# Kernel optimization log

Measured on AMD Instinct MI355X. Metric: run time of the kernel, lower is better.

The kernel has to match this reference:

```python
import jax, jax.numpy as jnp
import numpy as np

_CODESZ = 8   # E8 codeword dimension
_OFFSET = 0.25  # half-integer shift applied to D8 points


def _build_grid():
    # Faithful replication of get_grid(): cartesian product of arange(-4,4)
    # over 8 dims (torch.cartesian_prod order == 'ij' meshgrid, last dim fastest),
    # keep points with even coordinate sum and squared norm <= 10 (D8 subset),
    # then concat [d8 - 1/4, d8 + 1/4]. Yields 55650 codewords of dim 8.
    rng = np.arange(-4, 4, dtype=np.int8)
    pts = np.stack(np.meshgrid(*([rng] * _CODESZ), indexing='ij'), axis=-1).reshape(-1, _CODESZ)
    s = pts.sum(axis=-1, dtype=np.int16)
    n2 = (pts.astype(np.int16) * pts).sum(axis=-1)  # max 8*16 fits int16
    d8 = pts[(s % 2 == 0) & (n2 <= 10)].astype(np.float32)  # [27825, 8]
    grid = np.concatenate([d8 - _OFFSET, d8 + _OFFSET], axis=0)  # [55650, 8]
    grid_norm = (grid * grid).sum(axis=-1)  # diag(grid @ grid.T), [55650]
    return jnp.asarray(grid), jnp.asarray(grid_norm)


def setup_inputs() -> dict:
    key = jax.random.key(0)
    X = jax.random.normal(key, (8192, _CODESZ), dtype=jnp.float32)
    grid, grid_norm = _build_grid()
    return {"X": X, "grid": grid, "grid_norm": grid_norm}


def reference(X, grid, grid_norm):
    # quantize(X, return_idx=True):
    # nearest codeword under L2 <=> argmax of 2*X@g - ||g||^2
    scores = 2.0 * (X @ grid.T) - grid_norm          # [N, 55650]
    idx = jnp.argmax(scores, axis=-1)                # [N]
    vals = jnp.take(grid, idx, axis=0)               # [N, 8]
    idx_i16 = (idx + (-2 ** 15)).astype(jnp.int16)   # idx_offset + int16 cast
    return vals, idx_i16
```

## Files before the change

### kernel.cpp

```cpp
#include <hip/hip_runtime.h>
#include <math.h>


typedef short short8 __attribute__((ext_vector_type(8)));
typedef float f32x16 __attribute__((ext_vector_type(16)));

constexpr int NROWS  = 8192;
constexpr int NCW    = 55650;
constexpr int NT     = 1740;
constexpr int NCWP   = NT * 32;
constexpr int NCHUNK = 32;
constexpr int RBLK   = 32;

constexpr size_t OFF_GB = 0;
constexpr size_t OFF_XS = OFF_GB + (size_t)NCWP * 32;
constexpr size_t OFF_BK = OFF_XS + (size_t)NROWS * 64;

__device__ inline unsigned short bf16_rne(float f) {
  unsigned int u = __float_as_uint(f);
  unsigned int r = u + 0x7FFFu + ((u >> 16) & 1u);
  return (unsigned short)(r >> 16);
}
__device__ inline float bf16_f(unsigned short h) {
  return __uint_as_float(((unsigned int)h) << 16);
}
__device__ inline unsigned int enc_ord(float f) {
  unsigned int u = __float_as_uint(f);
  return (u & 0x80000000u) ? ~u : (u | 0x80000000u);
}
__device__ inline float dec_ord(unsigned int e) {
  unsigned int u = (e & 0x80000000u) ? (e & 0x7FFFFFFFu) : ~e;
  return __uint_as_float(u);
}
__device__ inline float max16(const f32x16& d) {
  float t1 = fmaxf(fmaxf(d[0], d[1]), d[2]);
  float t2 = fmaxf(fmaxf(d[3], d[4]), d[5]);
  float t3 = fmaxf(fmaxf(d[6], d[7]), d[8]);
  float t4 = fmaxf(fmaxf(d[9], d[10]), d[11]);
  float t5 = fmaxf(fmaxf(d[12], d[13]), d[14]);
  float u1 = fmaxf(fmaxf(t1, t2), t3);
  float u2 = fmaxf(fmaxf(t4, t5), d[15]);
  return fmaxf(u1, u2);
}

__global__ __launch_bounds__(256) void e8_prep(
    const float* __restrict__ X, const float* __restrict__ G,
    const float* __restrict__ GN, unsigned short* __restrict__ Gb,
    unsigned short* __restrict__ Xs, unsigned long long* __restrict__ best) {
  int i = blockIdx.x * 256 + threadIdx.x;
  if (i < NCWP) {
    unsigned short g16[16];
    if (i < NCW) {
      for (int j = 0; j < 8; ++j) g16[j] = bf16_rne(G[(size_t)i*8+j]);
      g16[8] = bf16_rne(GN[i]);
      for (int j = 9; j < 16; ++j) g16[j] = 0;
    } else {
      for (int j = 0; j < 8; ++j) g16[j] = 0;
      g16[8] = 0x7F7F;
      for (int j = 9; j < 16; ++j) g16[j] = 0;
    }
    uint4* dst = reinterpret_cast<uint4*>(Gb + (size_t)i * 16);
    dst[0] = *reinterpret_cast<uint4*>(&g16[0]);
    dst[1] = *reinterpret_cast<uint4*>(&g16[8]);
  } else if (i < NCWP + NROWS) {
    int r = i - NCWP;
    unsigned short hh[8], mm[8], ll[8], qq[8];
    for (int j = 0; j < 8; ++j) {
      float s = 2.0f * X[(size_t)r*8+j];
      unsigned short h = bf16_rne(s);  float r1 = s  - bf16_f(h);
      unsigned short m = bf16_rne(r1); float r2 = r1 - bf16_f(m);
      unsigned short l = bf16_rne(r2);
      hh[j] = h; mm[j] = m; ll[j] = l;
      qq[j] = (j == 0) ? (unsigned short)0xBF80 : 0;
    }
    uint4* dst = reinterpret_cast<uint4*>(Xs + (size_t)r * 32);
    dst[0] = *reinterpret_cast<uint4*>(hh);
    dst[1] = *reinterpret_cast<uint4*>(mm);
    dst[2] = *reinterpret_cast<uint4*>(ll);
    dst[3] = *reinterpret_cast<uint4*>(qq);
    best[r] = 0ull;
  }
}

__global__ __launch_bounds__(256, 4) void e8_main(
    const unsigned short* __restrict__ Gb,
    const unsigned short* __restrict__ Xs,
    unsigned long long* __restrict__ best) {
  const int lane = threadIdx.x & 63;
  const int wave = threadIdx.x >> 6;
  const int kg = lane >> 5, l31 = lane & 31;
  const int rowbase = blockIdx.x * 256 + wave * 64;

  short8 b10, b11, b20, b21;
  {
    const size_t row0 = (size_t)rowbase + l31;
    const size_t row1 = row0 + 32;
    b10 = *reinterpret_cast<const short8*>(Xs + (row0*4 + kg)*8);
    b20 = *reinterpret_cast<const short8*>(Xs + (row0*4 + 2 + kg)*8);
    b11 = *reinterpret_cast<const short8*>(Xs + (row1*4 + kg)*8);
    b21 = *reinterpret_cast<const short8*>(Xs + (row1*4 + 2 + kg)*8);
  }
  asm("" : "+v"(b10), "+v"(b11), "+v"(b20), "+v"(b21));

  const int ct0 = blockIdx.y * NT / NCHUNK;
  const int ct1 = (blockIdx.y + 1) * NT / NCHUNK;

  f32x16 cz;
#pragma unroll
  for (int i = 0; i < 16; ++i) cz[i] = 0.0f;

  float bs0 = -INFINITY, bs1 = -INFINITY;
  int   bi0 = 0,         bi1 = 0;

  const unsigned short* p = Gb + (size_t)ct0 * 512 + (size_t)l31 * 16;
  const int koff = kg << 3;

  short8 a1 = *reinterpret_cast<const short8*>(p);
  short8 a2 = *reinterpret_cast<const short8*>(p + koff);

  for (int ct = ct0; ct < ct1; ++ct) {
    p += 512;
    short8 na1 = *reinterpret_cast<const short8*>(p);
    short8 na2 = *reinterpret_cast<const short8*>(p + koff);

    f32x16 d0, d1;
    asm volatile(
        "v_mfma_f32_32x32x16_bf16 %0, %2, %4, %8\n\t"
        "v_mfma_f32_32x32x16_bf16 %1, %2, %5, %8\n\t"
        "v_mfma_f32_32x32x16_bf16 %0, %3, %6, %0\n\t"
        "v_mfma_f32_32x32x16_bf16 %1, %3, %7, %1\n\t"
        "s_nop 7\n\t"
        "s_nop 7"
        : "=&v"(d0), "=&v"(d1)
        : "v"(a1), "v"(a2), "v"(b10), "v"(b11), "v"(b20), "v"(b21), "v"(cz));

    const float m0 = max16(d0);
    const float m1 = max16(d1);
    bi0 = (m0 > bs0) ? ct : bi0;
    bs0 = fmaxf(bs0, m0);
    bi1 = (m1 > bs1) ? ct : bi1;
    bs1 = fmaxf(bs1, m1);
    a1 = na1; a2 = na2;
  }

  {
    unsigned long long key =
        ((unsigned long long)enc_ord(bs0) << 32) | (unsigned int)(~bi0);
    unsigned long long o = __shfl_xor(key, 32, 64);
    key = (o > key) ? o : key;
    if (lane < 32) atomicMax(&best[(size_t)rowbase + l31], key);
  }
  {
    unsigned long long key =
        ((unsigned long long)enc_ord(bs1) << 32) | (unsigned int)(~bi1);
    unsigned long long o = __shfl_xor(key, 32, 64);
    key = (o > key) ? o : key;
    if (lane < 32) atomicMax(&best[(size_t)rowbase + 32 + l31], key);
  }
}

__global__ __launch_bounds__(256) void e8_resolve(
    const unsigned short* __restrict__ Gb,
    const unsigned short* __restrict__ Xs, const float* __restrict__ G,
    const unsigned long long* __restrict__ best, float* __restrict__ out) {
  const int lane = threadIdx.x & 63;
  const int wave = threadIdx.x >> 6;
  const int kg = lane >> 5, l31 = lane & 31;
  const int rt = blockIdx.x;

  short8 b1, b2;
  {
    const size_t row = (size_t)rt * 32 + l31;
    b1 = *reinterpret_cast<const short8*>(Xs + (row*4 + kg)*8);
    b2 = *reinterpret_cast<const short8*>(Xs + (row*4 + 2 + kg)*8);
  }
  f32x16 cz;
#pragma unroll
  for (int i = 0; i < 16; ++i) cz[i] = 0.0f;

  for (int j = wave * 8; j < wave * 8 + 8; ++j) {
    const int srow = rt * 32 + j;
    const unsigned long long k = best[srow];
    const float sstar = dec_ord((unsigned int)(k >> 32));
    const int twin = (int)(~(unsigned int)(k & 0xFFFFFFFFull));

    const unsigned short* ga = Gb + (size_t)twin * 512 + (size_t)l31 * 16;
    short8 a1 = *reinterpret_cast<const short8*>(ga);
    short8 a2 = *reinterpret_cast<const short8*>(ga + (kg << 3));
    f32x16 d = __builtin_amdgcn_mfma_f32_32x32x16_bf16(a1, b1, cz, 0, 0, 0);
    d = __builtin_amdgcn_mfma_f32_32x32x16_bf16(a2, b2, d, 0, 0, 0);

    const int base = twin * 32 + 4 * kg;
    int cand = 0x7FFFFFFF;
#pragma unroll
    for (int r = 15; r >= 0; --r)
      cand = (d[r] == sstar) ? (base + ((r & 3) + 8 * (r >> 2))) : cand;
    if (l31 != j) cand = 0x7FFFFFFF;
    const int o = __shfl_xor(cand, 32, 64);
    cand = min(cand, o);
    if (lane == j) {
      const float4* g = reinterpret_cast<const float4*>(G + (size_t)cand * 8);
      float4 v0 = g[0], v1 = g[1];
      float4* od = reinterpret_cast<float4*>(out + (size_t)srow * 8);
      od[0] = v0; od[1] = v1;
      out[(size_t)NROWS * 8 + srow] = (float)(cand - 32768);
    }
  }
}

extern "C" void kernel_launch(void* const* d_in, const int* in_sizes, int n_in,
                              void* d_out, int out_size, void* d_ws, size_t ws_size,
                              hipStream_t stream) {
  const float* X  = (const float*)d_in[0];
  const float* G  = (const float*)d_in[1];
  const float* GN = (const float*)d_in[2];
  float* out = (float*)d_out;

  char* ws = (char*)d_ws;
  unsigned short*     Gb   = (unsigned short*)(ws + OFF_GB);
  unsigned short*     Xs   = (unsigned short*)(ws + OFF_XS);
  unsigned long long* best = (unsigned long long*)(ws + OFF_BK);

  e8_prep<<<(NCWP + NROWS + 255) / 256, 256, 0, stream>>>(X, G, GN, Gb, Xs, best);
  e8_main<<<dim3(RBLK, NCHUNK), 256, 0, stream>>>(Gb, Xs, best);
  e8_resolve<<<256, 256, 0, stream>>>(Gb, Xs, G, best, out);
}
```

Measured before the change: 46.01 us.

## Hand-schedule main loop in inline asm with group-of-8 max tracking

The main scoring loop becomes one hand-written inline-asm block per group of 8 codeword tiles. Double-buffered global loads and MFMAs on two accumulator sets are interleaved with elementwise v_max reductions, replacing the per-tile horizontal max16 and the s_nop padding. The best index is now tracked per 8-tile group instead of per tile, so the resolve kernel recomputes 8 tiles per row, and it launches twice as many blocks to compensate. The codeword padding, chunk count and occupancy hint also change. Hard-coded VGPR clobbers and manual waitcnt handling add correctness and register-pressure risk.

```diff
diff --git a/kernel.cpp b/kernel.cpp
--- a/kernel.cpp
+++ b/kernel.cpp
@@ -7,13 +7,14 @@
 
 constexpr int NROWS  = 8192;
 constexpr int NCW    = 55650;
-constexpr int NT     = 1740;
-constexpr int NCWP   = NT * 32;
-constexpr int NCHUNK = 32;
+constexpr int NT2    = 1744;
+constexpr int NG     = 218;
+constexpr int NCWP2  = NT2 * 32;
+constexpr int NCHUNK = 24;
 constexpr int RBLK   = 32;
 
 constexpr size_t OFF_GB = 0;
-constexpr size_t OFF_XS = OFF_GB + (size_t)NCWP * 32;
+constexpr size_t OFF_XS = OFF_GB + (size_t)NT2 * 1024;
 constexpr size_t OFF_BK = OFF_XS + (size_t)NROWS * 64;
 
 __device__ inline unsigned short bf16_rne(float f) {
@@ -31,16 +32,6 @@
 __device__ inline float dec_ord(unsigned int e) {
   unsigned int u = (e & 0x80000000u) ? (e & 0x7FFFFFFFu) : ~e;
   return __uint_as_float(u);
-}
-__device__ inline float max16(const f32x16& d) {
-  float t1 = fmaxf(fmaxf(d[0], d[1]), d[2]);
-  float t2 = fmaxf(fmaxf(d[3], d[4]), d[5]);
-  float t3 = fmaxf(fmaxf(d[6], d[7]), d[8]);
-  float t4 = fmaxf(fmaxf(d[9], d[10]), d[11]);
-  float t5 = fmaxf(fmaxf(d[12], d[13]), d[14]);
-  float u1 = fmaxf(fmaxf(t1, t2), t3);
-  float u2 = fmaxf(fmaxf(t4, t5), d[15]);
-  return fmaxf(u1, u2);
 }
 
 __global__ __launch_bounds__(256) void e8_prep(
@@ -48,7 +39,7 @@
     const float* __restrict__ GN, unsigned short* __restrict__ Gb,
     unsigned short* __restrict__ Xs, unsigned long long* __restrict__ best) {
   int i = blockIdx.x * 256 + threadIdx.x;
-  if (i < NCWP) {
+  if (i < NCWP2) {
     unsigned short g16[16];
     if (i < NCW) {
       for (int j = 0; j < 8; ++j) g16[j] = bf16_rne(G[(size_t)i*8+j]);
@@ -62,8 +53,8 @@
     uint4* dst = reinterpret_cast<uint4*>(Gb + (size_t)i * 16);
     dst[0] = *reinterpret_cast<uint4*>(&g16[0]);
     dst[1] = *reinterpret_cast<uint4*>(&g16[8]);
-  } else if (i < NCWP + NROWS) {
-    int r = i - NCWP;
+  } else if (i < NCWP2 + NROWS) {
+    int r = i - NCWP2;
     unsigned short hh[8], mm[8], ll[8], qq[8];
     for (int j = 0; j < 8; ++j) {
       float s = 2.0f * X[(size_t)r*8+j];
@@ -82,7 +73,95 @@
   }
 }
 
-__global__ __launch_bounds__(256, 4) void e8_main(
+#define MV(d, s) "v_mov_b32 v" #d ", v" #s "\n\t"
+#define MX(d, s) "v_max_f32 v" #d ", v" #d ", v" #s "\n\t"
+
+#define MOVA32 \
+  MV(128,64) MV(129,65) MV(130,66) MV(131,67) MV(132,68) MV(133,69) \
+  MV(134,70) MV(135,71) MV(136,72) MV(137,73) MV(138,74) MV(139,75) \
+  MV(140,76) MV(141,77) MV(142,78) MV(143,79) MV(144,80) MV(145,81) \
+  MV(146,82) MV(147,83) MV(148,84) MV(149,85) MV(150,86) MV(151,87) \
+  MV(152,88) MV(153,89) MV(154,90) MV(155,91) MV(156,92) MV(157,93) \
+  MV(158,94) MV(159,95)
+
+#define MAXA32 \
+  MX(128,64) MX(129,65) MX(130,66) MX(131,67) MX(132,68) MX(133,69) \
+  MX(134,70) MX(135,71) MX(136,72) MX(137,73) MX(138,74) MX(139,75) \
+  MX(140,76) MX(141,77) MX(142,78) MX(143,79) MX(144,80) MX(145,81) \
+  MX(146,82) MX(147,83) MX(148,84) MX(149,85) MX(150,86) MX(151,87) \
+  MX(152,88) MX(153,89) MX(154,90) MX(155,91) MX(156,92) MX(157,93) \
+  MX(158,94) MX(159,95)
+
+#define MAXB32 \
+  MX(128,96)  MX(129,97)  MX(130,98)  MX(131,99)  MX(132,100) MX(133,101) \
+  MX(134,102) MX(135,103) MX(136,104) MX(137,105) MX(138,106) MX(139,107) \
+  MX(140,108) MX(141,109) MX(142,110) MX(143,111) MX(144,112) MX(145,113) \
+  MX(146,114) MX(147,115) MX(148,116) MX(149,117) MX(150,118) MX(151,119) \
+  MX(152,120) MX(153,121) MX(154,122) MX(155,123) MX(156,124) MX(157,125) \
+  MX(158,126) MX(159,127)
+
+#define TREE \
+  MX(128,136) MX(129,137) MX(130,138) MX(131,139) \
+  MX(132,140) MX(133,141) MX(134,142) MX(135,143) \
+  MX(144,152) MX(145,153) MX(146,154) MX(147,155) \
+  MX(148,156) MX(149,157) MX(150,158) MX(151,159) \
+  MX(128,132) MX(129,133) MX(130,134) MX(131,135) \
+  MX(144,148) MX(145,149) MX(146,150) MX(147,151) \
+  MX(128,130) MX(129,131) MX(144,146) MX(145,147) \
+  MX(128,129) MX(144,145)
+
+#define TRACK \
+  "v_cmp_gt_f32 vcc, v128, v160\n\t" \
+  "v_cndmask_b32 v162, v162, %[gi], vcc\n\t" \
+  "v_max_f32 v160, v160, v128\n\t" \
+  "v_cmp_gt_f32 vcc, v144, v161\n\t" \
+  "v_cndmask_b32 v163, v163, %[gi], vcc\n\t" \
+  "v_max_f32 v161, v161, v144\n\t"
+
+#define TILE_A \
+  "s_waitcnt vmcnt(2)\n\t" \
+  "v_mfma_f32_32x32x16_bf16 v[64:79], v[56:59], %[b10], %[cz]\n\t" \
+  "v_mfma_f32_32x32x16_bf16 v[80:95], v[56:59], %[b11], %[cz]\n\t" \
+  "v_mfma_f32_32x32x16_bf16 v[64:79], v[60:63], %[b20], v[64:79]\n\t" \
+  "v_mfma_f32_32x32x16_bf16 v[80:95], v[60:63], %[b21], v[80:95]\n\t" \
+  "global_load_dwordx4 v[56:59], v46, %[gb]\n\t" \
+  "global_load_dwordx4 v[60:63], v47, %[gb]\n\t" \
+  "v_add_u32 v46, 0x400, v46\n\t" \
+  "v_add_u32 v47, 0x400, v47\n\t" \
+  "s_nop 1\n\t"
+
+#define TILE_B \
+  "s_waitcnt vmcnt(2)\n\t" \
+  "v_mfma_f32_32x32x16_bf16 v[96:111], v[48:51], %[b10], %[cz]\n\t" \
+  "v_mfma_f32_32x32x16_bf16 v[112:127], v[48:51], %[b11], %[cz]\n\t" \
+  "v_mfma_f32_32x32x16_bf16 v[96:111], v[52:55], %[b20], v[96:111]\n\t" \
+  "v_mfma_f32_32x32x16_bf16 v[112:127], v[52:55], %[b21], v[112:127]\n\t" \
+  "global_load_dwordx4 v[48:51], v46, %[gb]\n\t" \
+  "global_load_dwordx4 v[52:55], v47, %[gb]\n\t" \
+  "v_add_u32 v46, 0x400, v46\n\t" \
+  "v_add_u32 v47, 0x400, v47\n\t" \
+  "s_nop 1\n\t"
+
+#define GROUP_ASM \
+  TILE_A TILE_B MOVA32 TILE_A MAXB32 TILE_B MAXA32 \
+  TILE_A MAXB32 TILE_B MAXA32 TILE_A MAXB32 TILE_B MAXA32 \
+  "s_nop 1\n\t" MAXB32 TREE TRACK "s_nop 0"
+
+#define CLOBS \
+  "v46","v47","v48","v49","v50","v51","v52","v53","v54","v55", \
+  "v56","v57","v58","v59","v60","v61","v62","v63","v64","v65", \
+  "v66","v67","v68","v69","v70","v71","v72","v73","v74","v75", \
+  "v76","v77","v78","v79","v80","v81","v82","v83","v84","v85", \
+  "v86","v87","v88","v89","v90","v91","v92","v93","v94","v95", \
+  "v96","v97","v98","v99","v100","v101","v102","v103","v104","v105", \
+  "v106","v107","v108","v109","v110","v111","v112","v113","v114","v115", \
+  "v116","v117","v118","v119","v120","v121","v122","v123","v124","v125", \
+  "v126","v127","v128","v129","v130","v131","v132","v133","v134","v135", \
+  "v136","v137","v138","v139","v140","v141","v142","v143","v144","v145", \
+  "v146","v147","v148","v149","v150","v151","v152","v153","v154","v155", \
+  "v156","v157","v158","v159","v160","v161","v162","v163"
+
+__global__ __launch_bounds__(256, 3) void e8_main(
     const unsigned short* __restrict__ Gb,
     const unsigned short* __restrict__ Xs,
     unsigned long long* __restrict__ best) {
@@ -102,46 +181,51 @@
   }
   asm("" : "+v"(b10), "+v"(b11), "+v"(b20), "+v"(b21));
 
-  const int ct0 = blockIdx.y * NT / NCHUNK;
-  const int ct1 = (blockIdx.y + 1) * NT / NCHUNK;
-
   f32x16 cz;
 #pragma unroll
   for (int i = 0; i < 16; ++i) cz[i] = 0.0f;
 
-  float bs0 = -INFINITY, bs1 = -INFINITY;
-  int   bi0 = 0,         bi1 = 0;
-
-  const unsigned short* p = Gb + (size_t)ct0 * 512 + (size_t)l31 * 16;
-  const int koff = kg << 3;
-
-  short8 a1 = *reinterpret_cast<const short8*>(p);
-  short8 a2 = *reinterpret_cast<const short8*>(p + koff);
-
-  for (int ct = ct0; ct < ct1; ++ct) {
-    p += 512;
-    short8 na1 = *reinterpret_cast<const short8*>(p);
-    short8 na2 = *reinterpret_cast<const short8*>(p + koff);
-
-    f32x16 d0, d1;
-    asm volatile(
-        "v_mfma_f32_32x32x16_bf16 %0, %2, %4, %8\n\t"
-        "v_mfma_f32_32x32x16_bf16 %1, %2, %5, %8\n\t"
-        "v_mfma_f32_32x32x16_bf16 %0, %3, %6, %0\n\t"
-        "v_mfma_f32_32x32x16_bf16 %1, %3, %7, %1\n\t"
-        "s_nop 7\n\t"
-        "s_nop 7"
-        : "=&v"(d0), "=&v"(d1)
-        : "v"(a1), "v"(a2), "v"(b10), "v"(b11), "v"(b20), "v"(b21), "v"(cz));
-
-    const float m0 = max16(d0);
-    const float m1 = max16(d1);
-    bi0 = (m0 > bs0) ? ct : bi0;
-    bs0 = fmaxf(bs0, m0);
-    bi1 = (m1 > bs1) ? ct : bi1;
-    bs1 = fmaxf(bs1, m1);
-    a1 = na1; a2 = na2;
-  }
+  const int g0 = blockIdx.y * NG / NCHUNK;
+  const int g1 = (blockIdx.y + 1) * NG / NCHUNK;
+  const unsigned long long gbv = (unsigned long long)Gb;
+
+  unsigned voff1 = (unsigned)g0 * 8192u + (unsigned)l31 * 32u;
+  unsigned voff2 = voff1 + (unsigned)kg * 16u;
+
+  asm volatile(
+      "v_mov_b32 v46, %[o1]\n\t"
+      "v_mov_b32 v47, %[o2]\n\t"
+      "v_mov_b32 v160, 0xff800000\n\t"
+      "v_mov_b32 v161, 0xff800000\n\t"
+      "v_mov_b32 v162, 0\n\t"
+      "v_mov_b32 v163, 0\n\t"
+      "global_load_dwordx4 v[56:59], v46, %[gb]\n\t"
+      "global_load_dwordx4 v[60:63], v47, %[gb]\n\t"
+      "v_add_u32 v46, 0x400, v46\n\t"
+      "v_add_u32 v47, 0x400, v47\n\t"
+      "global_load_dwordx4 v[48:51], v46, %[gb]\n\t"
+      "global_load_dwordx4 v[52:55], v47, %[gb]\n\t"
+      "v_add_u32 v46, 0x400, v46\n\t"
+      "v_add_u32 v47, 0x400, v47\n\t"
+      "s_waitcnt vmcnt(0)"
+      :: [gb]"s"(gbv), [o1]"v"(voff1), [o2]"v"(voff2)
+      : CLOBS, "memory");
+
+  for (int g = g0; g < g1; ++g) {
+    asm volatile(GROUP_ASM
+        :: [gb]"s"(gbv), [gi]"v"(g), [b10]"v"(b10), [b11]"v"(b11),
+           [b20]"v"(b20), [b21]"v"(b21), [cz]"v"(cz)
+        : CLOBS, "vcc", "memory");
+  }
+
+  float bs0, bs1; int bi0, bi1;
+  asm volatile(
+      "s_waitcnt vmcnt(0)\n\t"
+      "v_mov_b32 %0, v160\n\t"
+      "v_mov_b32 %1, v161\n\t"
+      "v_mov_b32 %2, v162\n\t"
+      "v_mov_b32 %3, v163"
+      : "=v"(bs0), "=v"(bs1), "=v"(bi0), "=v"(bi1) :: "memory");
 
   {
     unsigned long long key =
@@ -166,7 +250,8 @@
   const int lane = threadIdx.x & 63;
   const int wave = threadIdx.x >> 6;
   const int kg = lane >> 5, l31 = lane & 31;
-  const int rt = blockIdx.x;
+  const int rt   = blockIdx.x >> 1;
+  const int half = blockIdx.x & 1;
 
   short8 b1, b2;
   {
@@ -178,23 +263,29 @@
 #pragma unroll
   for (int i = 0; i < 16; ++i) cz[i] = 0.0f;
 
-  for (int j = wave * 8; j < wave * 8 + 8; ++j) {
+  const int jbeg = half * 16 + wave * 4;
+  for (int j = jbeg; j < jbeg + 4; ++j) {
     const int srow = rt * 32 + j;
     const unsigned long long k = best[srow];
     const float sstar = dec_ord((unsigned int)(k >> 32));
-    const int twin = (int)(~(unsigned int)(k & 0xFFFFFFFFull));
-
-    const unsigned short* ga = Gb + (size_t)twin * 512 + (size_t)l31 * 16;
-    short8 a1 = *reinterpret_cast<const short8*>(ga);
-    short8 a2 = *reinterpret_cast<const short8*>(ga + (kg << 3));
-    f32x16 d = __builtin_amdgcn_mfma_f32_32x32x16_bf16(a1, b1, cz, 0, 0, 0);
-    d = __builtin_amdgcn_mfma_f32_32x32x16_bf16(a2, b2, d, 0, 0, 0);
-
-    const int base = twin * 32 + 4 * kg;
+    const int gwin = (int)(~(unsigned int)(k & 0xFFFFFFFFull));
+
+    const int tb = gwin * 8;
     int cand = 0x7FFFFFFF;
+    for (int tt = tb; tt < tb + 8; ++tt) {
+      const unsigned short* ga = Gb + (size_t)tt * 512 + (size_t)l31 * 16;
+      short8 a1 = *reinterpret_cast<const short8*>(ga);
+      short8 a2 = *reinterpret_cast<const short8*>(ga + (kg << 3));
+      f32x16 d = __builtin_amdgcn_mfma_f32_32x32x16_bf16(a1, b1, cz, 0, 0, 0);
+      d = __builtin_amdgcn_mfma_f32_32x32x16_bf16(a2, b2, d, 0, 0, 0);
+
+      int tc = 0x0FFFFFFF;
 #pragma unroll
-    for (int r = 15; r >= 0; --r)
-      cand = (d[r] == sstar) ? (base + ((r & 3) + 8 * (r >> 2))) : cand;
+      for (int r = 15; r >= 0; --r)
+        tc = (d[r] == sstar) ? ((r & 3) + 8 * (r >> 2)) : tc;
+      const int gidx = tt * 32 + 4 * kg + tc;
+      cand = (gidx < cand) ? gidx : cand;
+    }
     if (l31 != j) cand = 0x7FFFFFFF;
     const int o = __shfl_xor(cand, 32, 64);
     cand = min(cand, o);
@@ -221,7 +312,7 @@
   unsigned short*     Xs   = (unsigned short*)(ws + OFF_XS);
   unsigned long long* best = (unsigned long long*)(ws + OFF_BK);
 
-  e8_prep<<<(NCWP + NROWS + 255) / 256, 256, 0, stream>>>(X, G, GN, Gb, Xs, best);
+  e8_prep<<<(NCWP2 + NROWS) / 256, 256, 0, stream>>>(X, G, GN, Gb, Xs, best);
   e8_main<<<dim3(RBLK, NCHUNK), 256, 0, stream>>>(Gb, Xs, best);
-  e8_resolve<<<256, 256, 0, stream>>>(Gb, Xs, G, best, out);
-}
+  e8_resolve<<<512, 256, 0, stream>>>(Gb, Xs, G, best, out);
+}
```

Measured after the change: 47.37 us. 1.03x slower.

## Switch to 16x16x32 MFMA with hand-scheduled asm main loop and grouped max tracking

Applied to the files above, without the earlier changes.

The main kernel now uses the 16x16x32 bf16 MFMA over 16-codeword tiles instead of the 32x32x16 instruction, with K=32 holding the hi/mid/lo split of X. The loop is written as inline assembly with fixed registers, a double-buffered global load of the codebook, and max reductions interleaved with MFMAs. It tracks the best score per group of 8 tiles rather than per tile, which cuts compare/select work. The resolve kernel then rescans the 8 tiles of the winning group. The hard-coded VGPR use and manual s_waitcnt/s_nop scheduling risk hazards and register pressure conflicts with the compiler.

```diff
diff --git a/kernel.cpp b/kernel.cpp
--- a/kernel.cpp
+++ b/kernel.cpp
@@ -3,17 +3,18 @@
 
 
 typedef short short8 __attribute__((ext_vector_type(8)));
-typedef float f32x16 __attribute__((ext_vector_type(16)));
+typedef float f32x4  __attribute__((ext_vector_type(4)));
 
 constexpr int NROWS  = 8192;
 constexpr int NCW    = 55650;
-constexpr int NT     = 1740;
-constexpr int NCWP   = NT * 32;
+constexpr int NT16   = 3488;
+constexpr int NG     = 436;
+constexpr int NCWP2  = NT16 * 16;
 constexpr int NCHUNK = 32;
 constexpr int RBLK   = 32;
 
 constexpr size_t OFF_GB = 0;
-constexpr size_t OFF_XS = OFF_GB + (size_t)NCWP * 32;
+constexpr size_t OFF_XS = OFF_GB + (size_t)NCWP2 * 32;
 constexpr size_t OFF_BK = OFF_XS + (size_t)NROWS * 64;
 
 __device__ inline unsigned short bf16_rne(float f) {
@@ -31,16 +32,6 @@
 __device__ inline float dec_ord(unsigned int e) {
   unsigned int u = (e & 0x80000000u) ? (e & 0x7FFFFFFFu) : ~e;
   return __uint_as_float(u);
-}
-__device__ inline float max16(const f32x16& d) {
-  float t1 = fmaxf(fmaxf(d[0], d[1]), d[2]);
-  float t2 = fmaxf(fmaxf(d[3], d[4]), d[5]);
-  float t3 = fmaxf(fmaxf(d[6], d[7]), d[8]);
-  float t4 = fmaxf(fmaxf(d[9], d[10]), d[11]);
-  float t5 = fmaxf(fmaxf(d[12], d[13]), d[14]);
-  float u1 = fmaxf(fmaxf(t1, t2), t3);
-  float u2 = fmaxf(fmaxf(t4, t5), d[15]);
-  return fmaxf(u1, u2);
 }
 
 __global__ __launch_bounds__(256) void e8_prep(
@@ -48,7 +39,7 @@
     const float* __restrict__ GN, unsigned short* __restrict__ Gb,
     unsigned short* __restrict__ Xs, unsigned long long* __restrict__ best) {
   int i = blockIdx.x * 256 + threadIdx.x;
-  if (i < NCWP) {
+  if (i < NCWP2) {
     unsigned short g16[16];
     if (i < NCW) {
       for (int j = 0; j < 8; ++j) g16[j] = bf16_rne(G[(size_t)i*8+j]);
@@ -62,8 +53,8 @@
     uint4* dst = reinterpret_cast<uint4*>(Gb + (size_t)i * 16);
     dst[0] = *reinterpret_cast<uint4*>(&g16[0]);
     dst[1] = *reinterpret_cast<uint4*>(&g16[8]);
-  } else if (i < NCWP + NROWS) {
-    int r = i - NCWP;
+  } else if (i < NCWP2 + NROWS) {
+    int r = i - NCWP2;
     unsigned short hh[8], mm[8], ll[8], qq[8];
     for (int j = 0; j < 8; ++j) {
       float s = 2.0f * X[(size_t)r*8+j];
@@ -82,80 +73,141 @@
   }
 }
 
+#define MV(d, s) "v_mov_b32 v" #d ", v" #s "\n\t"
+#define MX(d, s) "v_max_f32 v" #d ", v" #d ", v" #s "\n\t"
+
+#define T16A \
+  "s_waitcnt vmcnt(1)\n\t" \
+  "v_mfma_f32_16x16x32_bf16 v[72:75],  v[44:47], v[56:59], v[52:55]\n\t" \
+  "v_mfma_f32_16x16x32_bf16 v[76:79],  v[44:47], v[60:63], v[52:55]\n\t" \
+  "v_mfma_f32_16x16x32_bf16 v[80:83],  v[44:47], v[64:67], v[52:55]\n\t" \
+  "v_mfma_f32_16x16x32_bf16 v[84:87],  v[44:47], v[68:71], v[52:55]\n\t" \
+  "global_load_dwordx4 v[44:47], v40, %[gb]\n\t" \
+  "v_add_u32 v40, 0x200, v40\n\t"
+
+#define T16B \
+  "s_waitcnt vmcnt(1)\n\t" \
+  "v_mfma_f32_16x16x32_bf16 v[88:91],   v[48:51], v[56:59], v[52:55]\n\t" \
+  "v_mfma_f32_16x16x32_bf16 v[92:95],   v[48:51], v[60:63], v[52:55]\n\t" \
+  "v_mfma_f32_16x16x32_bf16 v[96:99],   v[48:51], v[64:67], v[52:55]\n\t" \
+  "v_mfma_f32_16x16x32_bf16 v[100:103], v[48:51], v[68:71], v[52:55]\n\t" \
+  "global_load_dwordx4 v[48:51], v40, %[gb]\n\t" \
+  "v_add_u32 v40, 0x200, v40\n\t"
+
+#define MOV16 \
+  MV(104,72) MV(105,73) MV(106,74) MV(107,75) MV(108,76) MV(109,77) \
+  MV(110,78) MV(111,79) MV(112,80) MV(113,81) MV(114,82) MV(115,83) \
+  MV(116,84) MV(117,85) MV(118,86) MV(119,87)
+
+#define MAXA16 \
+  MX(104,72) MX(105,73) MX(106,74) MX(107,75) MX(108,76) MX(109,77) \
+  MX(110,78) MX(111,79) MX(112,80) MX(113,81) MX(114,82) MX(115,83) \
+  MX(116,84) MX(117,85) MX(118,86) MX(119,87)
+
+#define MAXB16 \
+  MX(104,88)  MX(105,89)  MX(106,90)  MX(107,91)  MX(108,92)  MX(109,93) \
+  MX(110,94)  MX(111,95)  MX(112,96)  MX(113,97)  MX(114,98)  MX(115,99) \
+  MX(116,100) MX(117,101) MX(118,102) MX(119,103)
+
+#define TREETRACK \
+  MX(104,105) MX(106,107) MX(108,109) MX(110,111) \
+  MX(112,113) MX(114,115) MX(116,117) MX(118,119) \
+  MX(104,106) MX(108,110) MX(112,114) MX(116,118) \
+  "v_cmp_gt_f32 vcc, v104, v120\n\t" \
+  "v_cndmask_b32 v124, v124, %[gi], vcc\n\t" \
+  "v_max_f32 v120, v120, v104\n\t" \
+  "v_cmp_gt_f32 vcc, v108, v121\n\t" \
+  "v_cndmask_b32 v125, v125, %[gi], vcc\n\t" \
+  "v_max_f32 v121, v121, v108\n\t" \
+  "v_cmp_gt_f32 vcc, v112, v122\n\t" \
+  "v_cndmask_b32 v126, v126, %[gi], vcc\n\t" \
+  "v_max_f32 v122, v122, v112\n\t" \
+  "v_cmp_gt_f32 vcc, v116, v123\n\t" \
+  "v_cndmask_b32 v127, v127, %[gi], vcc\n\t" \
+  "v_max_f32 v123, v123, v116\n\t"
+
+#define GROUP16 \
+  T16A T16B MOV16 T16A MAXB16 T16B MAXA16 \
+  T16A MAXB16 T16B MAXA16 T16A MAXB16 T16B MAXA16 \
+  "s_nop 7\n\t" "s_nop 7\n\t" MAXB16 TREETRACK "s_nop 0"
+
+#define CLOBS \
+  "v40","v41","v42","v43","v44","v45","v46","v47","v48","v49", \
+  "v50","v51","v52","v53","v54","v55","v56","v57","v58","v59", \
+  "v60","v61","v62","v63","v64","v65","v66","v67","v68","v69", \
+  "v70","v71","v72","v73","v74","v75","v76","v77","v78","v79", \
+  "v80","v81","v82","v83","v84","v85","v86","v87","v88","v89", \
+  "v90","v91","v92","v93","v94","v95","v96","v97","v98","v99", \
+  "v100","v101","v102","v103","v104","v105","v106","v107","v108","v109", \
+  "v110","v111","v112","v113","v114","v115","v116","v117","v118","v119", \
+  "v120","v121","v122","v123","v124","v125","v126","v127"
+
 __global__ __launch_bounds__(256, 4) void e8_main(
     const unsigned short* __restrict__ Gb,
     const unsigned short* __restrict__ Xs,
     unsigned long long* __restrict__ best) {
   const int lane = threadIdx.x & 63;
   const int wave = threadIdx.x >> 6;
-  const int kg = lane >> 5, l31 = lane & 31;
+  const int l15 = lane & 15, kg = lane >> 4;
   const int rowbase = blockIdx.x * 256 + wave * 64;
 
-  short8 b10, b11, b20, b21;
-  {
-    const size_t row0 = (size_t)rowbase + l31;
-    const size_t row1 = row0 + 32;
-    b10 = *reinterpret_cast<const short8*>(Xs + (row0*4 + kg)*8);
-    b20 = *reinterpret_cast<const short8*>(Xs + (row0*4 + 2 + kg)*8);
-    b11 = *reinterpret_cast<const short8*>(Xs + (row1*4 + kg)*8);
-    b21 = *reinterpret_cast<const short8*>(Xs + (row1*4 + 2 + kg)*8);
-  }
-  asm("" : "+v"(b10), "+v"(b11), "+v"(b20), "+v"(b21));
-
-  const int ct0 = blockIdx.y * NT / NCHUNK;
-  const int ct1 = (blockIdx.y + 1) * NT / NCHUNK;
-
-  f32x16 cz;
+  const int g0 = blockIdx.y * NG / NCHUNK;
+  const int g1 = (blockIdx.y + 1) * NG / NCHUNK;
+  const unsigned long long gbv = (unsigned long long)Gb;
+  const unsigned long long xsv = (unsigned long long)Xs;
+
+  unsigned avo = (unsigned)g0 * 4096u + (unsigned)l15 * 32u +
+                 (kg == 3 ? 16u : 0u);
+  unsigned bvo = (unsigned)(rowbase + l15) * 64u + (unsigned)kg * 16u;
+
+  asm volatile(
+      "v_mov_b32 v40, %[ao]\n\t"
+      "v_mov_b32 v52, 0\n\t" "v_mov_b32 v53, 0\n\t"
+      "v_mov_b32 v54, 0\n\t" "v_mov_b32 v55, 0\n\t"
+      "v_mov_b32 v120, 0xff800000\n\t" "v_mov_b32 v121, 0xff800000\n\t"
+      "v_mov_b32 v122, 0xff800000\n\t" "v_mov_b32 v123, 0xff800000\n\t"
+      "v_mov_b32 v124, 0\n\t" "v_mov_b32 v125, 0\n\t"
+      "v_mov_b32 v126, 0\n\t" "v_mov_b32 v127, 0\n\t"
+      "global_load_dwordx4 v[56:59], %[bo], %[xs]\n\t"
+      "global_load_dwordx4 v[60:63], %[bo], %[xs] offset:1024\n\t"
+      "global_load_dwordx4 v[64:67], %[bo], %[xs] offset:2048\n\t"
+      "global_load_dwordx4 v[68:71], %[bo], %[xs] offset:3072\n\t"
+      "global_load_dwordx4 v[44:47], v40, %[gb]\n\t"
+      "v_add_u32 v40, 0x200, v40\n\t"
+      "global_load_dwordx4 v[48:51], v40, %[gb]\n\t"
+      "v_add_u32 v40, 0x200, v40\n\t"
+      "s_waitcnt vmcnt(0)"
+      :: [gb]"s"(gbv), [xs]"s"(xsv), [ao]"v"(avo), [bo]"v"(bvo)
+      : CLOBS, "memory");
+
+  for (int g = g0; g < g1; ++g) {
+    asm volatile(GROUP16
+        :: [gb]"s"(gbv), [gi]"v"(g)
+        : CLOBS, "vcc", "memory");
+  }
+
+  float bs0, bs1, bs2, bs3; int bi0, bi1, bi2, bi3;
+  asm volatile(
+      "s_waitcnt vmcnt(0)\n\t"
+      "v_mov_b32 %0, v120\n\t" "v_mov_b32 %1, v121\n\t"
+      "v_mov_b32 %2, v122\n\t" "v_mov_b32 %3, v123\n\t"
+      "v_mov_b32 %4, v124\n\t" "v_mov_b32 %5, v125\n\t"
+      "v_mov_b32 %6, v126\n\t" "v_mov_b32 %7, v127"
+      : "=v"(bs0), "=v"(bs1), "=v"(bs2), "=v"(bs3),
+        "=v"(bi0), "=v"(bi1), "=v"(bi2), "=v"(bi3) :: "memory");
+
+  const float bsa[4] = {bs0, bs1, bs2, bs3};
+  const int   bia[4] = {bi0, bi1, bi2, bi3};
 #pragma unroll
-  for (int i = 0; i < 16; ++i) cz[i] = 0.0f;
-
-  float bs0 = -INFINITY, bs1 = -INFINITY;
-  int   bi0 = 0,         bi1 = 0;
-
-  const unsigned short* p = Gb + (size_t)ct0 * 512 + (size_t)l31 * 16;
-  const int koff = kg << 3;
-
-  short8 a1 = *reinterpret_cast<const short8*>(p);
-  short8 a2 = *reinterpret_cast<const short8*>(p + koff);
-
-  for (int ct = ct0; ct < ct1; ++ct) {
-    p += 512;
-    short8 na1 = *reinterpret_cast<const short8*>(p);
-    short8 na2 = *reinterpret_cast<const short8*>(p + koff);
-
-    f32x16 d0, d1;
-    asm volatile(
-        "v_mfma_f32_32x32x16_bf16 %0, %2, %4, %8\n\t"
-        "v_mfma_f32_32x32x16_bf16 %1, %2, %5, %8\n\t"
-        "v_mfma_f32_32x32x16_bf16 %0, %3, %6, %0\n\t"
-        "v_mfma_f32_32x32x16_bf16 %1, %3, %7, %1\n\t"
-        "s_nop 7\n\t"
-        "s_nop 7"
-        : "=&v"(d0), "=&v"(d1)
-        : "v"(a1), "v"(a2), "v"(b10), "v"(b11), "v"(b20), "v"(b21), "v"(cz));
-
-    const float m0 = max16(d0);
-    const float m1 = max16(d1);
-    bi0 = (m0 > bs0) ? ct : bi0;
-    bs0 = fmaxf(bs0, m0);
-    bi1 = (m1 > bs1) ? ct : bi1;
-    bs1 = fmaxf(bs1, m1);
-    a1 = na1; a2 = na2;
-  }
-
-  {
+  for (int t = 0; t < 4; ++t) {
     unsigned long long key =
-        ((unsigned long long)enc_ord(bs0) << 32) | (unsigned int)(~bi0);
-    unsigned long long o = __shfl_xor(key, 32, 64);
+        ((unsigned long long)enc_ord(bsa[t]) << 32) | (unsigned int)(~bia[t]);
+    unsigned long long o = __shfl_xor(key, 16, 64);
     key = (o > key) ? o : key;
-    if (lane < 32) atomicMax(&best[(size_t)rowbase + l31], key);
-  }
-  {
-    unsigned long long key =
-        ((unsigned long long)enc_ord(bs1) << 32) | (unsigned int)(~bi1);
-    unsigned long long o = __shfl_xor(key, 32, 64);
+    o = __shfl_xor(key, 32, 64);
     key = (o > key) ? o : key;
-    if (lane < 32) atomicMax(&best[(size_t)rowbase + 32 + l31], key);
+    if (lane < 16)
+      atomicMax(&best[(size_t)rowbase + t * 16 + l15], key);
   }
 }
 
@@ -165,39 +217,40 @@
     const unsigned long long* __restrict__ best, float* __restrict__ out) {
   const int lane = threadIdx.x & 63;
   const int wave = threadIdx.x >> 6;
-  const int kg = lane >> 5, l31 = lane & 31;
+  const int l15 = lane & 15, kg = lane >> 4;
   const int rt = blockIdx.x;
 
-  short8 b1, b2;
+  short8 b;
   {
-    const size_t row = (size_t)rt * 32 + l31;
-    b1 = *reinterpret_cast<const short8*>(Xs + (row*4 + kg)*8);
-    b2 = *reinterpret_cast<const short8*>(Xs + (row*4 + 2 + kg)*8);
-  }
-  f32x16 cz;
-#pragma unroll
-  for (int i = 0; i < 16; ++i) cz[i] = 0.0f;
-
-  for (int j = wave * 8; j < wave * 8 + 8; ++j) {
-    const int srow = rt * 32 + j;
+    const size_t row = (size_t)rt * 16 + l15;
+    b = *reinterpret_cast<const short8*>(Xs + (row*4 + kg)*8);
+  }
+  f32x4 cz = {0.f, 0.f, 0.f, 0.f};
+
+  for (int j = wave * 4; j < wave * 4 + 4; ++j) {
+    const int srow = rt * 16 + j;
     const unsigned long long k = best[srow];
     const float sstar = dec_ord((unsigned int)(k >> 32));
-    const int twin = (int)(~(unsigned int)(k & 0xFFFFFFFFull));
-
-    const unsigned short* ga = Gb + (size_t)twin * 512 + (size_t)l31 * 16;
-    short8 a1 = *reinterpret_cast<const short8*>(ga);
-    short8 a2 = *reinterpret_cast<const short8*>(ga + (kg << 3));
-    f32x16 d = __builtin_amdgcn_mfma_f32_32x32x16_bf16(a1, b1, cz, 0, 0, 0);
-    d = __builtin_amdgcn_mfma_f32_32x32x16_bf16(a2, b2, d, 0, 0, 0);
-
-    const int base = twin * 32 + 4 * kg;
+    const int gwin = (int)(~(unsigned int)(k & 0xFFFFFFFFull));
+
+    const int tb = gwin * 8;
     int cand = 0x7FFFFFFF;
+    for (int tt = tb; tt < tb + 8; ++tt) {
+      const unsigned short* ga =
+          Gb + (size_t)tt * 256 + (size_t)l15 * 16 + (kg == 3 ? 8 : 0);
+      short8 a = *reinterpret_cast<const short8*>(ga);
+      f32x4 d = __builtin_amdgcn_mfma_f32_16x16x32_bf16(a, b, cz, 0, 0, 0);
+
+      int tc = 0x0FFFFFFF;
 #pragma unroll
-    for (int r = 15; r >= 0; --r)
-      cand = (d[r] == sstar) ? (base + ((r & 3) + 8 * (r >> 2))) : cand;
-    if (l31 != j) cand = 0x7FFFFFFF;
-    const int o = __shfl_xor(cand, 32, 64);
-    cand = min(cand, o);
+      for (int r = 3; r >= 0; --r)
+        tc = (d[r] == sstar) ? r : tc;
+      const int gidx = tt * 16 + kg * 4 + tc;
+      cand = (gidx < cand) ? gidx : cand;
+    }
+    if (l15 != j) cand = 0x7FFFFFFF;
+    int o = __shfl_xor(cand, 16, 64); cand = min(cand, o);
+    o = __shfl_xor(cand, 32, 64);     cand = min(cand, o);
     if (lane == j) {
       const float4* g = reinterpret_cast<const float4*>(G + (size_t)cand * 8);
       float4 v0 = g[0], v1 = g[1];
@@ -221,7 +274,7 @@
   unsigned short*     Xs   = (unsigned short*)(ws + OFF_XS);
   unsigned long long* best = (unsigned long long*)(ws + OFF_BK);
 
-  e8_prep<<<(NCWP + NROWS + 255) / 256, 256, 0, stream>>>(X, G, GN, Gb, Xs, best);
+  e8_prep<<<(NCWP2 + NROWS + 255) / 256, 256, 0, stream>>>(X, G, GN, Gb, Xs, best);
   e8_main<<<dim3(RBLK, NCHUNK), 256, 0, stream>>>(Gb, Xs, best);
-  e8_resolve<<<256, 256, 0, stream>>>(Gb, Xs, G, best, out);
-}
+  e8_resolve<<<512, 256, 0, stream>>>(Gb, Xs, G, best, out);
+}
```

New measurement: 45.00 us. 1.02x faster.
